# Kernel optimization log

Hardware: AMD Instinct MI355X
Metric: run time of the kernel (lower is better)

## Reference

```python
import jax, jax.numpy as jnp
import numpy as np

N_NODES = 100000
N_EDGES = 1000000
D = 64
OUT = 64
EPS = 1e-5


def setup_inputs() -> dict:
    key = jax.random.key(0)
    k1, k2, k3, k4 = jax.random.split(key, 4)
    x = jax.random.normal(k1, (N_NODES, D), dtype=jnp.float32)
    edge_index = jax.random.randint(k2, (2, N_EDGES), 0, N_NODES, dtype=jnp.int64)
    # Linear(2*D, OUT): torch default init ~ U(-1/sqrt(fan_in), 1/sqrt(fan_in))
    bound = 1.0 / np.sqrt(2 * D)
    W = jax.random.uniform(k3, (2 * D, OUT), minval=-bound, maxval=bound, dtype=jnp.float32)
    b = jax.random.uniform(k4, (OUT,), minval=-bound, maxval=bound, dtype=jnp.float32)
    gamma = jnp.ones((OUT,), dtype=jnp.float32)
    beta = jnp.zeros((OUT,), dtype=jnp.float32)
    return {"x": x, "edge_index": edge_index, "W": W, "b": b, "gamma": gamma, "beta": beta}


def reference(x, edge_index, W, b, gamma, beta):
    row, col = edge_index[0], edge_index[1]
    # gather source features and scatter-add into destination nodes
    neighbor_sum = jax.ops.segment_sum(x[row], col, num_segments=x.shape[0])  # [N, D]
    h = jnp.concatenate([x, neighbor_sum], axis=-1)  # [N, 2D]
    h = h @ W + b  # [N, OUT]
    # LayerNorm over last dim
    mu = jnp.mean(h, axis=-1, keepdims=True)
    var = jnp.var(h, axis=-1, keepdims=True)
    h = (h - mu) * jax.lax.rsqrt(var + EPS) * gamma + beta
    return h
```

## Files before the change

### kernel.cpp

```cpp
#include <hip/hip_runtime.h>

#define NN 100000
#define NE 1000000
#define OUT_D 64
#define EPS 1e-5f

#define NB 196
#define COLS 512
#define BSTRIDE 6016
#define EPB 4096
#define NBLK1 245
#define NPROJ 1024

typedef __attribute__((ext_vector_type(8))) short bf16x8;
typedef __attribute__((ext_vector_type(4))) float f32x4;

static __device__ __forceinline__ unsigned short f2bf(float f) {
    unsigned u = __float_as_uint(f);
    u += 0x7FFFu + ((u >> 16) & 1u);
    return (unsigned short)(u >> 16);
}
static __device__ __forceinline__ float bf2f(unsigned short s) {
    return __uint_as_float((unsigned)s << 16);
}

__global__ __launch_bounds__(256) void mega_kernel(
    const float* __restrict__ x, const float* __restrict__ W,
    const int* __restrict__ ei, int* __restrict__ gcur, unsigned* __restrict__ gbuf,
    unsigned short* __restrict__ y1, unsigned short* __restrict__ y2)
{
    const int tid = threadIdx.x;
    const int lane = tid & 63;
    const int wv = tid >> 6;

    if (blockIdx.x < NBLK1) {
        __shared__ int lcnt[NB];
        __shared__ int loff[NB + 1];
        __shared__ int lbase[NB];
        __shared__ int lcur[NB];
        __shared__ int wpart[4];
        __shared__ unsigned lbuf[EPB];
        __shared__ unsigned char lbkt[EPB];
        const int e0 = blockIdx.x * EPB;

        int rows[16], cols[16];
        #pragma unroll
        for (int j = 0; j < 16; ++j) {
            const int e = e0 + j * 256 + tid;
            const bool v = e < NE;
            rows[j] = v ? ei[e] : 0;
            cols[j] = v ? ei[NE + e] : -1;
        }
        for (int i = tid; i < NB; i += 256) lcnt[i] = 0;
        __syncthreads();
        #pragma unroll
        for (int j = 0; j < 16; ++j)
            if (cols[j] >= 0) atomicAdd(&lcnt[cols[j] >> 9], 1);
        __syncthreads();
        {
            const int c = (tid < NB) ? lcnt[tid] : 0;
            int s = c;
            #pragma unroll
            for (int o = 1; o < 64; o <<= 1) { int t = __shfl_up(s, o); if (lane >= o) s += t; }
            if (lane == 63) wpart[wv] = s;
            __syncthreads();
            int woff = 0;
            for (int ww = 0; ww < wv; ++ww) woff += wpart[ww];
            if (tid < NB) {
                loff[tid] = woff + s - c;
                lcur[tid] = woff + s - c;
                lbase[tid] = atomicAdd(&gcur[tid], c);
            }
            if (tid == NB - 1) loff[NB] = woff + s;
        }
        __syncthreads();
        #pragma unroll
        for (int j = 0; j < 16; ++j) {
            if (cols[j] >= 0) {
                const int b = cols[j] >> 9;
                const int p = atomicAdd(&lcur[b], 1);
                lbuf[p] = ((unsigned)rows[j] << 9) | (unsigned)(cols[j] & (COLS - 1));
                lbkt[p] = (unsigned char)b;
            }
        }
        __syncthreads();
        const int total = loff[NB];
        for (int t = tid; t < total; t += 256) {
            const int b = lbkt[t];
            const unsigned idx = (unsigned)(lbase[b] + (t - loff[b]));
            if (idx < BSTRIDE) gbuf[(size_t)b * BSTRIDE + idx] = lbuf[t];
        }
    } else {
        const int m = lane & 15;
        const int quad = lane >> 4;
        bf16x8 Wf[8][2];
        #pragma unroll
        for (int t = 0; t < 8; ++t)
            #pragma unroll
            for (int q = 0; q < 2; ++q) {
                bf16x8 f;
                #pragma unroll
                for (int j = 0; j < 8; ++j) {
                    const int k = q * 32 + quad * 8 + j;
                    const int krow = (t < 4) ? k : (64 + k);
                    const int col = (t & 3) * 16 + m;
                    f[j] = (short)f2bf(W[krow * 64 + col]);
                }
                Wf[t][q] = f;
            }
        for (int tile = (blockIdx.x - NBLK1) * 4 + wv; tile < NN / 16; tile += NPROJ * 4) {
            const int n0 = tile * 16;
            bf16x8 Af[2];
            #pragma unroll
            for (int q = 0; q < 2; ++q) {
                const float* px = x + (size_t)(n0 + m) * 64 + q * 32 + quad * 8;
                const f32x4 a0 = *(const f32x4*)px;
                const f32x4 a1 = *(const f32x4*)(px + 4);
                bf16x8 f;
                #pragma unroll
                for (int j = 0; j < 4; ++j) { f[j] = (short)f2bf(a0[j]); f[4 + j] = (short)f2bf(a1[j]); }
                Af[q] = f;
            }
            #pragma unroll
            for (int t = 0; t < 8; ++t) {
                f32x4 acc = {0.f, 0.f, 0.f, 0.f};
                acc = __builtin_amdgcn_mfma_f32_16x16x32_bf16(Af[0], Wf[t][0], acc, 0, 0, 0);
                acc = __builtin_amdgcn_mfma_f32_16x16x32_bf16(Af[1], Wf[t][1], acc, 0, 0, 0);
                unsigned short* __restrict__ dst = (t < 4) ? y1 : y2;
                const int colb = (t & 3) * 16 + m;
                #pragma unroll
                for (int r = 0; r < 4; ++r)
                    dst[(size_t)(n0 + quad * 4 + r) * 64 + colb] = f2bf(acc[r]);
            }
        }
    }
}

__global__ __launch_bounds__(256) void place_kernel(
    const int* __restrict__ gcur, const unsigned* __restrict__ gbuf,
    int* __restrict__ csr, int* __restrict__ rowptr)
{
    __shared__ int cofs[COLS];
    __shared__ int ccur[COLS];
    __shared__ int sbase[2];
    __shared__ unsigned lsrc[BSTRIDE];
    __shared__ unsigned ldst[BSTRIDE];
    const int b = blockIdx.x, tid = threadIdx.x;
    const int n0 = b << 9;

    if (tid < 64) {
        int partial = 0;
        for (int i = tid; i < b; i += 64) partial += gcur[i];
        #pragma unroll
        for (int o = 32; o; o >>= 1) partial += __shfl_xor(partial, o);
        if (tid == 0) { sbase[0] = partial; sbase[1] = min(gcur[b], BSTRIDE); }
    }
    for (int i = tid; i < COLS; i += 256) cofs[i] = 0;
    __syncthreads();
    const int base = sbase[0], cntE = sbase[1];
    const unsigned* __restrict__ gb = gbuf + (size_t)b * BSTRIDE;

    for (int i = tid; i < cntE; i += 256) {
        const unsigned p = gb[i];
        lsrc[i] = p;
        atomicAdd(&cofs[p & (COLS - 1)], 1);
    }
    __syncthreads();
    if (tid < 64) {
        int v[8], tsum = 0;
        #pragma unroll
        for (int k = 0; k < 8; ++k) { v[k] = cofs[tid * 8 + k]; tsum += v[k]; }
        int s = tsum;
        #pragma unroll
        for (int o = 1; o < 64; o <<= 1) { int t = __shfl_up(s, o); if (tid >= o) s += t; }
        int run = s - tsum;
        #pragma unroll
        for (int k = 0; k < 8; ++k) { cofs[tid * 8 + k] = run; ccur[tid * 8 + k] = run; run += v[k]; }
    }
    __syncthreads();
    for (int i = tid; i < cntE; i += 256) {
        const unsigned p = lsrc[i];
        const int pos = atomicAdd(&ccur[p & (COLS - 1)], 1);
        ldst[pos] = p >> 9;
    }
    __syncthreads();
    for (int i = tid; i < cntE; i += 256) csr[base + i] = (int)ldst[i];
    const int ncols = min(COLS, NN - n0);
    for (int c = tid; c < ncols; c += 256) rowptr[n0 + c] = base + cofs[c];
    if (b == NB - 1 && tid == 0) rowptr[NN] = base + cntE;
}

__global__ __launch_bounds__(256) void out_kernel(
    const int* __restrict__ rowptr, const int* __restrict__ csr,
    const unsigned short* __restrict__ y1, const unsigned short* __restrict__ y2,
    const float* __restrict__ bias, const float* __restrict__ gamma,
    const float* __restrict__ beta, float* __restrict__ out)
{
    const int lane = threadIdx.x & 63;
    const int n = __builtin_amdgcn_readfirstlane(blockIdx.x * 4 + (threadIdx.x >> 6));
    const int s0 = rowptr[n], s1 = rowptr[n + 1];

    float acc = bf2f(y1[(size_t)n * OUT_D + lane]) + bias[lane];
    int i = s0;
    for (; i + 4 <= s1; i += 4) {
        const int r0 = csr[i], r1 = csr[i + 1], r2 = csr[i + 2], r3 = csr[i + 3];
        const float v0 = bf2f(y2[(size_t)r0 * OUT_D + lane]);
        const float v1 = bf2f(y2[(size_t)r1 * OUT_D + lane]);
        const float v2 = bf2f(y2[(size_t)r2 * OUT_D + lane]);
        const float v3 = bf2f(y2[(size_t)r3 * OUT_D + lane]);
        acc += (v0 + v1) + (v2 + v3);
    }
    for (; i < s1; ++i) acc += bf2f(y2[(size_t)csr[i] * OUT_D + lane]);

    float sv = acc, sq = acc * acc;
    #pragma unroll
    for (int off = 32; off; off >>= 1) { sv += __shfl_xor(sv, off); sq += __shfl_xor(sq, off); }
    const float mu  = sv * (1.0f / OUT_D);
    const float var = sq * (1.0f / OUT_D) - mu * mu;
    const float inv = rsqrtf(var + EPS);
    out[(size_t)n * OUT_D + lane] = (acc - mu) * inv * gamma[lane] + beta[lane];
}

extern "C" void kernel_launch(void* const* d_in, const int* in_sizes, int n_in,
                              void* d_out, int out_size, void* d_ws, size_t ws_size,
                              hipStream_t stream) {
    const float* x     = (const float*)d_in[0];
    const int*   ei    = (const int*)  d_in[1];
    const float* W     = (const float*)d_in[2];
    const float* b     = (const float*)d_in[3];
    const float* gamma = (const float*)d_in[4];
    const float* beta  = (const float*)d_in[5];
    float* out = (float*)d_out;

    char* p = (char*)d_ws;
    int*            gcur   = (int*)p;             p += 1024;
    unsigned*       gbuf   = (unsigned*)p;        p += (size_t)NB * BSTRIDE * 4;
    int*            csr    = (int*)p;             p += (size_t)NE * 4;
    int*            rowptr = (int*)p;             p += (NB * COLS + 64) * 4;
    unsigned short* y1     = (unsigned short*)p;  p += (size_t)NN * OUT_D * 2;
    unsigned short* y2     = (unsigned short*)p;

    hipMemsetAsync(gcur, 0, NB * sizeof(int), stream);
    mega_kernel <<<NBLK1 + NPROJ, 256, 0, stream>>>(x, W, ei, gcur, gbuf, y1, y2);
    place_kernel<<<NB, 256, 0, stream>>>(gcur, gbuf, csr, rowptr);
    out_kernel  <<<NN / 4, 256, 0, stream>>>(rowptr, csr, y1, y2, b, gamma, beta, out);
}
```

Measured before the change: 150.1 us.

## Pad CSR rows to multiples of four with dummy zero node, vectorize index loads

Per-column CSR segments are padded to a multiple of 4, with padding entries pointing at an extra zero row appended to y2. Each bucket now gets a fixed-stride CSR region, so the cross-block prefix sum over gcur is dropped. Row start and length are packed into one 32-bit word, so out_kernel reads one value instead of two. The gather loop reads indices as int4 vectors and unrolls to 8 neighbours with no scalar tail. The cost is extra padded gathers of the zero row and a larger shared-memory buffer, and row lengths are capped at 511 in the packed format.

Measured after the change: 143.4 us. -4.5%, faster.

```diff
diff --git a/kernel.cpp b/kernel.cpp
--- a/kernel.cpp
+++ b/kernel.cpp
@@ -8,12 +8,14 @@
 #define NB 196
 #define COLS 512
 #define BSTRIDE 6016
+#define PBSTRIDE 8064
 #define EPB 4096
 #define NBLK1 245
 #define NPROJ 1024
 
 typedef __attribute__((ext_vector_type(8))) short bf16x8;
 typedef __attribute__((ext_vector_type(4))) float f32x4;
+typedef __attribute__((ext_vector_type(4))) int i32x4;
 
 static __device__ __forceinline__ unsigned short f2bf(float f) {
     unsigned u = __float_as_uint(f);
@@ -138,26 +140,22 @@
 
 __global__ __launch_bounds__(256) void place_kernel(
     const int* __restrict__ gcur, const unsigned* __restrict__ gbuf,
-    int* __restrict__ csr, int* __restrict__ rowptr)
+    int* __restrict__ csr, unsigned* __restrict__ rowpack,
+    unsigned short* __restrict__ y2)
 {
-    __shared__ int cofs[COLS];
+    __shared__ int cofs[COLS + 1];
     __shared__ int ccur[COLS];
-    __shared__ int sbase[2];
     __shared__ unsigned lsrc[BSTRIDE];
-    __shared__ unsigned ldst[BSTRIDE];
+    __shared__ int ldst[PBSTRIDE];
     const int b = blockIdx.x, tid = threadIdx.x;
     const int n0 = b << 9;
 
-    if (tid < 64) {
-        int partial = 0;
-        for (int i = tid; i < b; i += 64) partial += gcur[i];
-        #pragma unroll
-        for (int o = 32; o; o >>= 1) partial += __shfl_xor(partial, o);
-        if (tid == 0) { sbase[0] = partial; sbase[1] = min(gcur[b], BSTRIDE); }
-    }
+    if (b == 0 && tid < 64) y2[(size_t)NN * OUT_D + tid] = 0;
+
     for (int i = tid; i < COLS; i += 256) cofs[i] = 0;
-    __syncthreads();
-    const int base = sbase[0], cntE = sbase[1];
+    for (int i = tid; i < PBSTRIDE; i += 256) ldst[i] = NN;
+    __syncthreads();
+    const int cntE = min(gcur[b], BSTRIDE);
     const unsigned* __restrict__ gb = gbuf + (size_t)b * BSTRIDE;
 
     for (int i = tid; i < cntE; i += 256) {
@@ -169,48 +167,69 @@
     if (tid < 64) {
         int v[8], tsum = 0;
         #pragma unroll
-        for (int k = 0; k < 8; ++k) { v[k] = cofs[tid * 8 + k]; tsum += v[k]; }
+        for (int k = 0; k < 8; ++k) { v[k] = (cofs[tid * 8 + k] + 3) & ~3; tsum += v[k]; }
         int s = tsum;
         #pragma unroll
         for (int o = 1; o < 64; o <<= 1) { int t = __shfl_up(s, o); if (tid >= o) s += t; }
         int run = s - tsum;
         #pragma unroll
         for (int k = 0; k < 8; ++k) { cofs[tid * 8 + k] = run; ccur[tid * 8 + k] = run; run += v[k]; }
+        if (tid == 63) cofs[COLS] = run;
     }
     __syncthreads();
     for (int i = tid; i < cntE; i += 256) {
         const unsigned p = lsrc[i];
         const int pos = atomicAdd(&ccur[p & (COLS - 1)], 1);
-        ldst[pos] = p >> 9;
-    }
-    __syncthreads();
-    for (int i = tid; i < cntE; i += 256) csr[base + i] = (int)ldst[i];
+        ldst[pos] = (int)(p >> 9);
+    }
+    __syncthreads();
+    const int ptotal = cofs[COLS];
+    const int base = b * PBSTRIDE;
+    for (int i = tid; i < ptotal; i += 256) csr[base + i] = ldst[i];
     const int ncols = min(COLS, NN - n0);
-    for (int c = tid; c < ncols; c += 256) rowptr[n0 + c] = base + cofs[c];
-    if (b == NB - 1 && tid == 0) rowptr[NN] = base + cntE;
+    for (int c = tid; c < ncols; c += 256) {
+        const int st = cofs[c];
+        const int len = min(cofs[c + 1] - st, 511);
+        rowpack[n0 + c] = ((unsigned)st << 9) | (unsigned)len;
+    }
 }
 
 __global__ __launch_bounds__(256) void out_kernel(
-    const int* __restrict__ rowptr, const int* __restrict__ csr,
+    const unsigned* __restrict__ rowpack, const int* __restrict__ csr,
     const unsigned short* __restrict__ y1, const unsigned short* __restrict__ y2,
     const float* __restrict__ bias, const float* __restrict__ gamma,
     const float* __restrict__ beta, float* __restrict__ out)
 {
     const int lane = threadIdx.x & 63;
     const int n = __builtin_amdgcn_readfirstlane(blockIdx.x * 4 + (threadIdx.x >> 6));
-    const int s0 = rowptr[n], s1 = rowptr[n + 1];
+    const unsigned pk = rowpack[n];
+    const int cnt = (int)(pk & 511);
+    const i32x4* __restrict__ cs =
+        (const i32x4*)(csr + (n >> 9) * PBSTRIDE + (int)(pk >> 9));
 
     float acc = bf2f(y1[(size_t)n * OUT_D + lane]) + bias[lane];
-    int i = s0;
-    for (; i + 4 <= s1; i += 4) {
-        const int r0 = csr[i], r1 = csr[i + 1], r2 = csr[i + 2], r3 = csr[i + 3];
-        const float v0 = bf2f(y2[(size_t)r0 * OUT_D + lane]);
-        const float v1 = bf2f(y2[(size_t)r1 * OUT_D + lane]);
-        const float v2 = bf2f(y2[(size_t)r2 * OUT_D + lane]);
-        const float v3 = bf2f(y2[(size_t)r3 * OUT_D + lane]);
+    int i = 0;
+    for (; i + 8 <= cnt; i += 8) {
+        const i32x4 c0 = cs[(i >> 2)];
+        const i32x4 c1 = cs[(i >> 2) + 1];
+        const float v0 = bf2f(y2[(size_t)c0[0] * OUT_D + lane]);
+        const float v1 = bf2f(y2[(size_t)c0[1] * OUT_D + lane]);
+        const float v2 = bf2f(y2[(size_t)c0[2] * OUT_D + lane]);
+        const float v3 = bf2f(y2[(size_t)c0[3] * OUT_D + lane]);
+        const float v4 = bf2f(y2[(size_t)c1[0] * OUT_D + lane]);
+        const float v5 = bf2f(y2[(size_t)c1[1] * OUT_D + lane]);
+        const float v6 = bf2f(y2[(size_t)c1[2] * OUT_D + lane]);
+        const float v7 = bf2f(y2[(size_t)c1[3] * OUT_D + lane]);
+        acc += ((v0 + v1) + (v2 + v3)) + ((v4 + v5) + (v6 + v7));
+    }
+    if (i < cnt) {
+        const i32x4 c0 = cs[(i >> 2)];
+        const float v0 = bf2f(y2[(size_t)c0[0] * OUT_D + lane]);
+        const float v1 = bf2f(y2[(size_t)c0[1] * OUT_D + lane]);
+        const float v2 = bf2f(y2[(size_t)c0[2] * OUT_D + lane]);
+        const float v3 = bf2f(y2[(size_t)c0[3] * OUT_D + lane]);
         acc += (v0 + v1) + (v2 + v3);
     }
-    for (; i < s1; ++i) acc += bf2f(y2[(size_t)csr[i] * OUT_D + lane]);
 
     float sv = acc, sq = acc * acc;
     #pragma unroll
@@ -233,15 +252,15 @@
     float* out = (float*)d_out;
 
     char* p = (char*)d_ws;
-    int*            gcur   = (int*)p;             p += 1024;
-    unsigned*       gbuf   = (unsigned*)p;        p += (size_t)NB * BSTRIDE * 4;
-    int*            csr    = (int*)p;             p += (size_t)NE * 4;
-    int*            rowptr = (int*)p;             p += (NB * COLS + 64) * 4;
-    unsigned short* y1     = (unsigned short*)p;  p += (size_t)NN * OUT_D * 2;
-    unsigned short* y2     = (unsigned short*)p;
+    int*            gcur    = (int*)p;             p += 1024;
+    unsigned*       gbuf    = (unsigned*)p;        p += (size_t)NB * BSTRIDE * 4;
+    int*            csr     = (int*)p;             p += (size_t)NB * PBSTRIDE * 4;
+    unsigned*       rowpack = (unsigned*)p;        p += (size_t)(NB * COLS) * 4;
+    unsigned short* y1      = (unsigned short*)p;  p += (size_t)NN * OUT_D * 2;
+    unsigned short* y2      = (unsigned short*)p;
 
     hipMemsetAsync(gcur, 0, NB * sizeof(int), stream);
     mega_kernel <<<NBLK1 + NPROJ, 256, 0, stream>>>(x, W, ei, gcur, gbuf, y1, y2);
-    place_kernel<<<NB, 256, 0, stream>>>(gcur, gbuf, csr, rowptr);
-    out_kernel  <<<NN / 4, 256, 0, stream>>>(rowptr, csr, y1, y2, b, gamma, beta, out);
-}
+    place_kernel<<<NB, 256, 0, stream>>>(gcur, gbuf, csr, rowpack, y2);
+    out_kernel  <<<NN / 4, 256, 0, stream>>>(rowpack, csr, y1, y2, b, gamma, beta, out);
+}
```
